# Performance work log

Hardware: AMD Instinct MI355X
Metric: run time of the kernel (lower is better)

The kernel has to match this reference:

```python
import jax, jax.numpy as jnp
import numpy as np

D = 256        # embedding dim (params[0])
V = 50000      # candidate vocab (params[1])
VW = 200000    # word vocab
B = 1024       # number of entities (batched ragged loop)
C = 64         # candidates per side (padded fixed length)
TOP_K = 10     # params[2]


def setup_inputs() -> dict:
    key = jax.random.key(0)
    ks = jax.random.split(key, 10)
    return {
        "word_l_ids": jax.random.randint(ks[0], (B,), 0, VW),
        "word_r_ids": jax.random.randint(ks[1], (B,), 0, VW),
        "cand_l_ids": jax.random.randint(ks[2], (B, C), 0, V),
        "cand_r_ids": jax.random.randint(ks[3], (B, C), 0, V),
        "word_embeds": jax.random.normal(ks[4], (VW, D), dtype=jnp.float32) * 0.1,
        "candidate_embeds": jax.random.normal(ks[5], (V, D), dtype=jnp.float32) * 0.1,
        # truncated_normal(stddev=0.5) for W_a, stddev=1.0 for W_c
        "W_a": jax.random.truncated_normal(ks[6], -2.0, 2.0, (D, D), dtype=jnp.float32) * 0.5,
        "b_a": jnp.zeros((1, D), dtype=jnp.float32),
        "W_c": jax.random.truncated_normal(ks[7], -2.0, 2.0, (2 * D, D), dtype=jnp.float32),
        "b_c": jnp.zeros((1, D), dtype=jnp.float32),
    }


def reference(word_l_ids, word_r_ids, cand_l_ids, cand_r_ids,
              word_embeds, candidate_embeds, W_a, b_a, W_c, b_c):
    # per-entity embedding lookups
    wl = word_embeds[word_l_ids]            # [B, D]
    wr = word_embeds[word_r_ids]            # [B, D]
    cl = candidate_embeds[cand_l_ids]       # [B, C, D]
    cr = candidate_embeds[cand_r_ids]       # [B, C, D]

    def attend(word, cands):
        # embed_word_align = tanh(word @ W_a + b_a)
        align = jnp.tanh(word @ W_a + b_a)                       # [B, D]
        # softmax over candidate axis (axis=0 in original per-entity view)
        scores = jnp.einsum("bcd,bd->bc", cands, align)          # [B, C]
        att = jax.nn.softmax(scores, axis=-1)                    # [B, C]
        # weighted sum of candidate embeddings
        return jnp.einsum("bc,bcd->bd", att, cands)              # [B, D]

    # note: left aggregation attends over RIGHT candidates and vice versa
    aggre_l = attend(wl, cr)
    aggre_r = attend(wr, cl)

    words_whole = wl + wr
    cands_whole = aggre_r + aggre_l
    phrase = jnp.tanh(jnp.concatenate([words_whole, cands_whole], axis=-1) @ W_c + b_c)  # [B, D]

    logits = phrase @ candidate_embeds.T    # [B, V]
    y_pred = jax.nn.softmax(logits, axis=-1)
    _, top_candidates = jax.lax.top_k(y_pred, TOP_K)             # [B, TOP_K]
    return y_pred, top_candidates
```

## Files before the change

kernel.cpp:

```cpp
#include <hip/hip_runtime.h>
#include <math.h>

#define DD 256
#define BB 1024
#define CC 64
#define VV 50000
#define TOPK 10
#define BM 128
#define BN 128
#define BK 64
#define LDK 72
#define NCHUNK 391
#define NMBLK 8
#define NWG (NCHUNK * NMBLK)
#define MAXCAND 60

typedef __attribute__((ext_vector_type(8))) short bf16x8;
typedef __attribute__((ext_vector_type(4))) float f32x4;

__device__ inline unsigned short f2bf(float x) {
    unsigned u = __float_as_uint(x);
    unsigned r = (u + 0x7FFFu + ((u >> 16) & 1u)) >> 16;
    return (unsigned short)r;
}

__global__ __launch_bounds__(256) void k_prep(
    const float* __restrict__ CE, unsigned short* __restrict__ CEb)
{
    const int i = blockIdx.x * 256 + threadIdx.x;
    const size_t base = (size_t)i * 8;
    if (base >= (size_t)VV * DD) return;
    const float4 a = *(const float4*)(CE + base);
    const float4 b = *(const float4*)(CE + base + 4);
    uint4 o;
    o.x = (unsigned)f2bf(a.x) | ((unsigned)f2bf(a.y) << 16);
    o.y = (unsigned)f2bf(a.z) | ((unsigned)f2bf(a.w) << 16);
    o.z = (unsigned)f2bf(b.x) | ((unsigned)f2bf(b.y) << 16);
    o.w = (unsigned)f2bf(b.z) | ((unsigned)f2bf(b.w) << 16);
    *(uint4*)(CEb + base) = o;
}

__global__ __launch_bounds__(256) void k_phrase(
    const int* __restrict__ wl_ids, const int* __restrict__ wr_ids,
    const int* __restrict__ cl_ids, const int* __restrict__ cr_ids,
    const float* __restrict__ WE, const float* __restrict__ CE,
    const float* __restrict__ W_a, const float* __restrict__ b_a,
    const float* __restrict__ W_c, const float* __restrict__ b_c,
    float* __restrict__ phrase, unsigned short* __restrict__ phraseb)
{
    const int b = blockIdx.x;
    const int t = threadIdx.x;
    __shared__ float s_wl[DD], s_wr[DD], s_align[DD], s_agg0[DD], s_agg1[DD];
    __shared__ float s_part[256];
    __shared__ float s_att[CC];
    __shared__ int s_rid[CC];

    s_wl[t] = WE[(size_t)wl_ids[b] * DD + t];
    s_wr[t] = WE[(size_t)wr_ids[b] * DD + t];
    __syncthreads();

    for (int side = 0; side < 2; ++side) {
        const float* w    = (side == 0) ? s_wl : s_wr;
        const int*   cids = (side == 0) ? (cr_ids + b * CC) : (cl_ids + b * CC);

        float acc = b_a[t];
        #pragma unroll 4
        for (int k = 0; k < DD; ++k) acc = fmaf(w[k], W_a[k * DD + t], acc);
        s_align[t] = tanhf(acc);
        if (t < CC) s_rid[t] = cids[t];
        __syncthreads();

        {
            const int c = t & 63, p = t >> 6;
            const float* crow = CE + (size_t)s_rid[c] * DD + p * 64;
            const float* al = s_align + p * 64;
            float sc = 0.f;
            #pragma unroll 4
            for (int j = 0; j < 64; ++j) sc = fmaf(crow[j], al[j], sc);
            s_part[t] = sc;
        }
        __syncthreads();
        if (t < CC) {
            float s = s_part[t] + s_part[64 + t] + s_part[128 + t] + s_part[192 + t];
            float m = s;
            for (int off = 32; off; off >>= 1) m = fmaxf(m, __shfl_xor(m, off, 64));
            float e = expf(s - m);
            float sum = e;
            for (int off = 32; off; off >>= 1) sum += __shfl_xor(sum, off, 64);
            s_att[t] = e / sum;
        }
        __syncthreads();
        {
            float ag = 0.f;
            #pragma unroll 4
            for (int c = 0; c < CC; ++c)
                ag = fmaf(s_att[c], CE[(size_t)s_rid[c] * DD + t], ag);
            if (side == 0) s_agg0[t] = ag; else s_agg1[t] = ag;
        }
        __syncthreads();
    }

    s_wl[t]  += s_wr[t];
    s_agg0[t] += s_agg1[t];
    __syncthreads();

    float acc = b_c[t];
    #pragma unroll 4
    for (int k = 0; k < DD; ++k) acc = fmaf(s_wl[k],  W_c[k * DD + t], acc);
    #pragma unroll 4
    for (int k = 0; k < DD; ++k) acc = fmaf(s_agg0[k], W_c[(DD + k) * DD + t], acc);
    const float ph = tanhf(acc);
    phrase[b * DD + t] = ph;
    phraseb[b * DD + t] = f2bf(ph);
}

__global__ __launch_bounds__(256) void k_align(
    const int* __restrict__ wl_ids, const int* __restrict__ wr_ids,
    const float* __restrict__ WE,
    const float* __restrict__ W_a, const float* __restrict__ b_a,
    float* __restrict__ alignbuf, float* __restrict__ wordsum)
{
    __shared__ float sA[32][260];
    __shared__ int s_id[32];

    const int t  = threadIdx.x;
    const int rt = blockIdx.x >> 2;
    const int cg = blockIdx.x & 3;
    const int b0 = rt * 16;
    const int s0 = rt * 32;

    if (t < 32) {
        const int e = b0 + (t >> 1);
        s_id[t] = (t & 1) ? wr_ids[e] : wl_ids[e];
    }
    __syncthreads();

    #pragma unroll 8
    for (int r = 0; r < 32; ++r)
        sA[r][t] = WE[(size_t)s_id[r] * DD + t];
    __syncthreads();

    if (cg == 0) {
        #pragma unroll
        for (int i = 0; i < 16; ++i)
            wordsum[(size_t)(b0 + i) * DD + t] = sA[2 * i][t] + sA[2 * i + 1][t];
    }

    const int c = t & 63, mg = t >> 6;
    const int col = cg * 64 + c;
    const float ba = b_a[col];
    float acc[8];
    #pragma unroll
    for (int j = 0; j < 8; ++j) acc[j] = ba;

    for (int k4 = 0; k4 < 64; ++k4) {
        const int kb = k4 * 4;
        const float w0 = W_a[(size_t)(kb + 0) * DD + col];
        const float w1 = W_a[(size_t)(kb + 1) * DD + col];
        const float w2 = W_a[(size_t)(kb + 2) * DD + col];
        const float w3 = W_a[(size_t)(kb + 3) * DD + col];
        #pragma unroll
        for (int j = 0; j < 8; ++j) {
            const float4 a = *(const float4*)&sA[mg * 8 + j][kb];
            acc[j] = fmaf(a.x, w0, acc[j]);
            acc[j] = fmaf(a.y, w1, acc[j]);
            acc[j] = fmaf(a.z, w2, acc[j]);
            acc[j] = fmaf(a.w, w3, acc[j]);
        }
    }
    #pragma unroll
    for (int j = 0; j < 8; ++j)
        alignbuf[(size_t)(s0 + mg * 8 + j) * DD + col] = tanhf(acc[j]);
}

__global__ __launch_bounds__(256) void k_attn(
    const int* __restrict__ cl_ids, const int* __restrict__ cr_ids,
    const float* __restrict__ CE, const float* __restrict__ alignbuf,
    float* __restrict__ aggsum)
{
    __shared__ float sC[CC][260];
    __shared__ float sAl[DD];
    __shared__ float s_part[256];
    __shared__ float s_att[CC];
    __shared__ int s_rid[CC];

    const int b = blockIdx.x;
    const int t = threadIdx.x;
    float agg_acc = 0.f;

    for (int side = 0; side < 2; ++side) {
        const int* cids = (side == 0) ? (cr_ids + b * CC) : (cl_ids + b * CC);
        if (t < CC) s_rid[t] = cids[t];
        sAl[t] = alignbuf[(size_t)(2 * b + side) * DD + t];
        __syncthreads();

        #pragma unroll 8
        for (int r = 0; r < CC; ++r)
            sC[r][t] = CE[(size_t)s_rid[r] * DD + t];
        __syncthreads();

        {
            const int c = t & 63, p = t >> 6;
            float sc = 0.f;
            #pragma unroll
            for (int jj = 0; jj < 16; ++jj) {
                const float4 v  = *(const float4*)&sC[c][p * 64 + 4 * jj];
                const float4 al = *(const float4*)&sAl[p * 64 + 4 * jj];
                sc = fmaf(v.x, al.x, sc);
                sc = fmaf(v.y, al.y, sc);
                sc = fmaf(v.z, al.z, sc);
                sc = fmaf(v.w, al.w, sc);
            }
            s_part[t] = sc;
        }
        __syncthreads();
        if (t < CC) {
            float s = s_part[t] + s_part[64 + t] + s_part[128 + t] + s_part[192 + t];
            float m = s;
            for (int off = 32; off; off >>= 1) m = fmaxf(m, __shfl_xor(m, off, 64));
            float e = expf(s - m);
            float sum = e;
            for (int off = 32; off; off >>= 1) sum += __shfl_xor(sum, off, 64);
            s_att[t] = e / sum;
        }
        __syncthreads();
        {
            float ag = 0.f;
            #pragma unroll 8
            for (int c = 0; c < CC; ++c)
                ag = fmaf(s_att[c], sC[c][t], ag);
            agg_acc += ag;
        }
        __syncthreads();
    }
    aggsum[(size_t)b * DD + t] = agg_acc;
}

__global__ __launch_bounds__(256) void k_phrase2(
    const float* __restrict__ wordsum, const float* __restrict__ aggsum,
    const float* __restrict__ W_c, const float* __restrict__ b_c,
    float* __restrict__ phrase, unsigned short* __restrict__ phraseb)
{
    __shared__ float sX[16][516];

    const int t  = threadIdx.x;
    const int rt = blockIdx.x >> 2;
    const int cg = blockIdx.x & 3;
    const int b0 = rt * 16;

    #pragma unroll
    for (int i = 0; i < 16; ++i) {
        sX[i][t]       = wordsum[(size_t)(b0 + i) * DD + t];
        sX[i][DD + t]  = aggsum [(size_t)(b0 + i) * DD + t];
    }
    __syncthreads();

    const int c = t & 63, mg = t >> 6;
    const int col = cg * 64 + c;
    const float bc = b_c[col];
    float acc[4];
    #pragma unroll
    for (int j = 0; j < 4; ++j) acc[j] = bc;

    for (int k4 = 0; k4 < 128; ++k4) {
        const int kb = k4 * 4;
        const float w0 = W_c[(size_t)(kb + 0) * DD + col];
        const float w1 = W_c[(size_t)(kb + 1) * DD + col];
        const float w2 = W_c[(size_t)(kb + 2) * DD + col];
        const float w3 = W_c[(size_t)(kb + 3) * DD + col];
        #pragma unroll
        for (int j = 0; j < 4; ++j) {
            const float4 a = *(const float4*)&sX[mg * 4 + j][kb];
            acc[j] = fmaf(a.x, w0, acc[j]);
            acc[j] = fmaf(a.y, w1, acc[j]);
            acc[j] = fmaf(a.z, w2, acc[j]);
            acc[j] = fmaf(a.w, w3, acc[j]);
        }
    }
    #pragma unroll
    for (int j = 0; j < 4; ++j) {
        const int b = b0 + mg * 4 + j;
        const float ph = tanhf(acc[j]);
        phrase[(size_t)b * DD + col] = ph;
        phraseb[(size_t)b * DD + col] = f2bf(ph);
    }
}

template<bool STATS, bool BF16CE>
__global__ __launch_bounds__(256) void k_gemm(
    const unsigned short* __restrict__ phraseb,
    const float* __restrict__ CE, const unsigned short* __restrict__ CEb,
    float* __restrict__ out,
    float* __restrict__ pmax, float* __restrict__ psum,
    const float* __restrict__ rowM, const float* __restrict__ rowInvS,
    const float* __restrict__ rowTh,
    int* __restrict__ cand_idx, int* __restrict__ cand_cnt)
{
    __shared__ __align__(16) char smem_raw[BM * LDK * 2 * 2];
    unsigned short* sA = (unsigned short*)smem_raw;
    unsigned short* sB = sA + BM * LDK;

    const int t = threadIdx.x;
    const int wave = t >> 6, lane = t & 63;
    const int wm = wave >> 1, wn = wave & 1;
    const int quad = lane >> 4, l15 = lane & 15;

    const int wg = blockIdx.x;
    const int q  = (wg & 7) * NCHUNK + (wg >> 3);
    const int m0 = (q & 7) * BM;
    const int cn = q >> 3;
    const int n0 = cn * BN;

    f32x4 acc[4][4] = {};

    for (int k0 = 0; k0 < DD; k0 += BK) {
        __syncthreads();
        #pragma unroll
        for (int r = 0; r < 4; ++r) {
            const int idx = t + r * 256;
            const int m = idx >> 3, k8 = (idx & 7) * 8;
            const uint4 v = *(const uint4*)(phraseb + (size_t)(m0 + m) * DD + k0 + k8);
            *(uint4*)(sA + m * LDK + k8) = v;
        }
        if constexpr (BF16CE) {
            #pragma unroll
            for (int r = 0; r < 4; ++r) {
                const int idx = t + r * 256;
                const int n = idx >> 3, k8 = (idx & 7) * 8;
                const int gn = n0 + n;
                uint4 v = make_uint4(0u, 0u, 0u, 0u);
                if (gn < VV) v = *(const uint4*)(CEb + (size_t)gn * DD + k0 + k8);
                *(uint4*)(sB + n * LDK + k8) = v;
            }
        } else {
            #pragma unroll
            for (int r = 0; r < 8; ++r) {
                const int idx = t + r * 256;
                const int n = idx >> 4, k4 = (idx & 15) * 4;
                const int gn = n0 + n;
                float4 v = make_float4(0.f, 0.f, 0.f, 0.f);
                if (gn < VV) v = *(const float4*)(CE + (size_t)gn * DD + k0 + k4);
                ushort4 h;
                h.x = f2bf(v.x); h.y = f2bf(v.y); h.z = f2bf(v.z); h.w = f2bf(v.w);
                *(ushort4*)(sB + n * LDK + k4) = h;
            }
        }
        __syncthreads();
        #pragma unroll
        for (int kk = 0; kk < BK; kk += 32) {
            bf16x8 af[4], bfr[4];
            #pragma unroll
            for (int i = 0; i < 4; ++i) {
                af[i]  = *(const bf16x8*)(sA + (wm * 64 + i * 16 + l15) * LDK + kk + quad * 8);
                bfr[i] = *(const bf16x8*)(sB + (wn * 64 + i * 16 + l15) * LDK + kk + quad * 8);
            }
            #pragma unroll
            for (int i = 0; i < 4; ++i)
                #pragma unroll
                for (int j = 0; j < 4; ++j)
                    acc[i][j] = __builtin_amdgcn_mfma_f32_16x16x32_bf16(af[i], bfr[j], acc[i][j], 0, 0, 0);
        }
    }

    bool val[4];
    #pragma unroll
    for (int j = 0; j < 4; ++j) val[j] = (n0 + wn * 64 + j * 16 + l15) < VV;

    if constexpr (STATS) {
        __shared__ float sM[2][BM], sS[2][BM];
        #pragma unroll
        for (int i = 0; i < 4; ++i) {
            #pragma unroll
            for (int r = 0; r < 4; ++r) {
                float m1 = -INFINITY;
                #pragma unroll
                for (int j = 0; j < 4; ++j) if (val[j]) m1 = fmaxf(m1, acc[i][j][r]);
                #pragma unroll
                for (int off = 8; off >= 1; off >>= 1) m1 = fmaxf(m1, __shfl_xor(m1, off, 64));
                float s = 0.f;
                #pragma unroll
                for (int j = 0; j < 4; ++j) if (val[j]) s += __expf(acc[i][j][r] - m1);
                #pragma unroll
                for (int off = 8; off >= 1; off >>= 1) s += __shfl_xor(s, off, 64);
                if (l15 == 0) {
                    const int mloc = wm * 64 + i * 16 + quad * 4 + r;
                    sM[wn][mloc] = m1;
                    sS[wn][mloc] = s;
                }
            }
        }
        __syncthreads();
        if (t < BM) {
            const float Ma = sM[0][t], Mb = sM[1][t];
            const float nM = fmaxf(Ma, Mb);
            const float S  = sS[0][t] * __expf(Ma - nM) + sS[1][t] * __expf(Mb - nM);
            const size_t o = (size_t)(m0 + t) * NCHUNK + cn;
            pmax[o] = nM;
            psum[o] = S;
        }
    } else {
        __shared__ float sMr[BM], sIr[BM], sTr[BM];
        if (t < BM) {
            sMr[t] = rowM[m0 + t];
            sIr[t] = rowInvS[m0 + t];
            sTr[t] = rowTh[m0 + t];
        }
        float* stage = (float*)smem_raw;
        #pragma unroll
        for (int h = 0; h < 4; ++h) {
            __syncthreads();
            if (wm == (h >> 1)) {
                const int ibase = (h & 1) * 2;
                #pragma unroll
                for (int ii = 0; ii < 2; ++ii) {
                    const int i = ibase + ii;
                    #pragma unroll
                    for (int r = 0; r < 4; ++r) {
                        const int ml = wm * 64 + i * 16 + quad * 4 + r;
                        const int rl = ii * 16 + quad * 4 + r;
                        const float M = sMr[ml], inv = sIr[ml], th = sTr[ml];
                        #pragma unroll
                        for (int j = 0; j < 4; ++j) {
                            const float y = __expf(acc[i][j][r] - M) * inv;
                            stage[rl * 132 + wn * 64 + j * 16 + l15] = y;
                            if (val[j] && y >= th) {
                                const int gm = m0 + ml;
                                const int gn = n0 + wn * 64 + j * 16 + l15;
                                const int p = atomicAdd(&cand_cnt[gm], 1);
                                if (p < MAXCAND) cand_idx[gm * MAXCAND + p] = gn;
                            }
                        }
                    }
                }
            }
            __syncthreads();
            #pragma unroll
            for (int k = 0; k < 4; ++k) {
                const int f = t + k * 256;
                const int row = f >> 5, c4 = f & 31;
                const int gcol = n0 + c4 * 4;
                if (gcol + 3 < VV) {
                    const f32x4 v = *(const f32x4*)&stage[row * 132 + c4 * 4];
                    __builtin_nontemporal_store(v,
                        (f32x4*)(out + (size_t)(m0 + h * 32 + row) * VV + gcol));
                }
            }
        }
    }
}

__global__ __launch_bounds__(64) void k_rowstats(
    const float* __restrict__ pmax, const float* __restrict__ psum,
    float* __restrict__ rowM, float* __restrict__ rowInvS, float* __restrict__ rowTh,
    int* __restrict__ cand_cnt)
{
    const int b = blockIdx.x, t = threadIdx.x;
    float M = -INFINITY, S = 0.f;
    float top[TOPK];
    #pragma unroll
    for (int j = 0; j < TOPK; ++j) top[j] = -INFINITY;

    for (int c = t; c < NCHUNK; c += 64) {
        const float m = pmax[(size_t)b * NCHUNK + c];
        const float s = psum[(size_t)b * NCHUNK + c];
        const float nM = fmaxf(M, m);
        S = S * __expf(M - nM) + s * __expf(m - nM);
        M = nM;
        if (m > top[TOPK - 1]) {
            float v = m;
            #pragma unroll
            for (int p = 0; p < TOPK; ++p) {
                const float hi = fmaxf(top[p], v), lo = fminf(top[p], v);
                top[p] = hi; v = lo;
            }
        }
    }
    #pragma unroll
    for (int off = 32; off; off >>= 1) {
        const float m2 = __shfl_xor(M, off, 64);
        const float s2 = __shfl_xor(S, off, 64);
        const float nM = fmaxf(M, m2);
        S = S * __expf(M - nM) + s2 * __expf(m2 - nM);
        M = nM;
    }
    float v10 = -INFINITY;
    for (int k = 0; k < TOPK; ++k) {
        float g = top[0];
        #pragma unroll
        for (int off = 32; off; off >>= 1) g = fmaxf(g, __shfl_xor(g, off, 64));
        v10 = g;
        const unsigned long long mk = __ballot(top[0] == g);
        if (mk && t == __ffsll(mk) - 1) {
            #pragma unroll
            for (int p = 0; p < TOPK - 1; ++p) top[p] = top[p + 1];
            top[TOPK - 1] = -INFINITY;
        }
    }
    if (t == 0) {
        rowM[b] = M;
        const float inv = 1.f / S;
        rowInvS[b] = inv;
        rowTh[b] = 0.90f * __expf(v10 - M) * inv;
        cand_cnt[b] = 0;
    }
}

__global__ __launch_bounds__(64) void k_rescore(
    const float* __restrict__ phrase, const float* __restrict__ CE,
    const int* __restrict__ cand_idx, const int* __restrict__ cand_cnt,
    float* __restrict__ topk_out)
{
    const int b = blockIdx.x, lane = threadIdx.x;
    int cnt = cand_cnt[b];
    if (cnt > MAXCAND) cnt = MAXCAND;
    __shared__ float s_val[MAXCAND];
    __shared__ int   s_idx[MAXCAND];

    if (lane < MAXCAND) { s_val[lane] = -INFINITY; s_idx[lane] = 0x7ffffff0; }
    __syncthreads();

    const float4 ph = *(const float4*)(phrase + (size_t)b * DD + lane * 4);
    for (int c = 0; c < cnt; ++c) {
        const int id = cand_idx[b * MAXCAND + c];
        const float4 ce = *(const float4*)(CE + (size_t)id * DD + lane * 4);
        float d = ph.x * ce.x + ph.y * ce.y + ph.z * ce.z + ph.w * ce.w;
        #pragma unroll
        for (int off = 32; off; off >>= 1) d += __shfl_xor(d, off, 64);
        if (lane == 0) { s_val[c] = d; s_idx[c] = id; }
    }
    __syncthreads();
    if (lane == 0) {
        for (int j = 0; j < TOPK; ++j) {
            int best = j;
            for (int c = j + 1; c < cnt; ++c) {
                if (s_val[c] > s_val[best] ||
                    (s_val[c] == s_val[best] && s_idx[c] < s_idx[best])) best = c;
            }
            const float bv = s_val[best]; const int bi = s_idx[best];
            s_val[best] = s_val[j]; s_idx[best] = s_idx[j];
            s_val[j] = bv; s_idx[j] = bi;
            topk_out[b * TOPK + j] = (float)bi;
        }
    }
}

extern "C" void kernel_launch(void* const* d_in, const int* in_sizes, int n_in,
                              void* d_out, int out_size, void* d_ws, size_t ws_size,
                              hipStream_t stream) {
    const int*   wl_ids = (const int*)d_in[0];
    const int*   wr_ids = (const int*)d_in[1];
    const int*   cl_ids = (const int*)d_in[2];
    const int*   cr_ids = (const int*)d_in[3];
    const float* WE     = (const float*)d_in[4];
    const float* CE     = (const float*)d_in[5];
    const float* W_a    = (const float*)d_in[6];
    const float* b_a    = (const float*)d_in[7];
    const float* W_c    = (const float*)d_in[8];
    const float* b_c    = (const float*)d_in[9];

    float* out = (float*)d_out;
    float* ws  = (float*)d_ws;

    float* phrase  = ws;
    unsigned short* phraseb = (unsigned short*)(ws + 262144);
    float* pmax    = ws + 262144 + 131072;
    float* psum    = pmax + (size_t)BB * NCHUNK;
    float* rowM    = psum + (size_t)BB * NCHUNK;
    float* rowInvS = rowM + BB;
    float* rowTh   = rowInvS + BB;
    int*   cand_idx = (int*)(rowTh + BB);
    int*   cand_cnt = cand_idx + (size_t)BB * MAXCAND;
    float* topk_out = out + (size_t)BB * VV;

    const size_t baseBytes = (size_t)((char*)(cand_cnt + BB) - (char*)ws);

    float* alignbuf = (float*)((char*)ws + baseBytes);
    float* wordsum  = alignbuf + (size_t)2 * BB * DD;
    float* aggsum   = wordsum + (size_t)BB * DD;
    const size_t ext1End = baseBytes + (size_t)4 * BB * DD * 4;
    const bool newphrase = ws_size >= ext1End;

    const size_t ceOff = ((newphrase ? ext1End : baseBytes) + 255) & ~(size_t)255;
    const bool bf16ce = ws_size >= ceOff + (size_t)VV * DD * 2;
    unsigned short* CEb = (unsigned short*)((char*)ws + ceOff);

    if (newphrase) {
        k_align<<<256, 256, 0, stream>>>(wl_ids, wr_ids, WE, W_a, b_a, alignbuf, wordsum);
        k_attn<<<BB, 256, 0, stream>>>(cl_ids, cr_ids, CE, alignbuf, aggsum);
        k_phrase2<<<256, 256, 0, stream>>>(wordsum, aggsum, W_c, b_c, phrase, phraseb);
    } else {
        k_phrase<<<BB, 256, 0, stream>>>(wl_ids, wr_ids, cl_ids, cr_ids,
                                         WE, CE, W_a, b_a, W_c, b_c, phrase, phraseb);
    }
    if (bf16ce) {
        k_prep<<<(VV * DD / 8 + 255) / 256, 256, 0, stream>>>(CE, CEb);
        k_gemm<true, true><<<NWG, 256, 0, stream>>>(phraseb, CE, CEb, out,
            pmax, psum, rowM, rowInvS, rowTh, cand_idx, cand_cnt);
        k_rowstats<<<BB, 64, 0, stream>>>(pmax, psum, rowM, rowInvS, rowTh, cand_cnt);
        k_gemm<false, true><<<NWG, 256, 0, stream>>>(phraseb, CE, CEb, out,
            pmax, psum, rowM, rowInvS, rowTh, cand_idx, cand_cnt);
    } else {
        k_gemm<true, false><<<NWG, 256, 0, stream>>>(phraseb, CE, CEb, out,
            pmax, psum, rowM, rowInvS, rowTh, cand_idx, cand_cnt);
        k_rowstats<<<BB, 64, 0, stream>>>(pmax, psum, rowM, rowInvS, rowTh, cand_cnt);
        k_gemm<false, false><<<NWG, 256, 0, stream>>>(phraseb, CE, CEb, out,
            pmax, psum, rowM, rowInvS, rowTh, cand_idx, cand_cnt);
    }
    k_rescore<<<BB, 64, 0, stream>>>(phrase, CE, cand_idx, cand_cnt, topk_out);
}
```

Before: 642.2 us.

## Replace second GEMM pass with local-max exp write and per-row rescale

The GEMM now runs once. It writes exp(logit - chunk max) to the output along with per-chunk max and sum, and a new k_scale kernel rescales each row in place by exp(chunk max - row max)/S while collecting top-k candidates. This removes the recomputed GEMM but adds a full read and write of the 200MB output. Separately, the attention kernel is split per side, reads candidates straight from global memory instead of staging them in LDS, and stores its result in alignbuf, which removes aggsum.

```diff
diff --git a/kernel.cpp b/kernel.cpp
--- a/kernel.cpp
+++ b/kernel.cpp
@@ -14,6 +14,7 @@
 #define NMBLK 8
 #define NWG (NCHUNK * NMBLK)
 #define MAXCAND 60
+#define QLEN 12500
 
 typedef __attribute__((ext_vector_type(8))) short bf16x8;
 typedef __attribute__((ext_vector_type(4))) float f32x4;
@@ -175,69 +176,59 @@
 
 __global__ __launch_bounds__(256) void k_attn(
     const int* __restrict__ cl_ids, const int* __restrict__ cr_ids,
-    const float* __restrict__ CE, const float* __restrict__ alignbuf,
-    float* __restrict__ aggsum)
-{
-    __shared__ float sC[CC][260];
+    const float* __restrict__ CE, float* __restrict__ alignbuf)
+{
     __shared__ float sAl[DD];
     __shared__ float s_part[256];
     __shared__ float s_att[CC];
     __shared__ int s_rid[CC];
 
-    const int b = blockIdx.x;
+    const int bid = blockIdx.x;
+    const int b = bid >> 1, side = bid & 1;
     const int t = threadIdx.x;
-    float agg_acc = 0.f;
-
-    for (int side = 0; side < 2; ++side) {
-        const int* cids = (side == 0) ? (cr_ids + b * CC) : (cl_ids + b * CC);
-        if (t < CC) s_rid[t] = cids[t];
-        sAl[t] = alignbuf[(size_t)(2 * b + side) * DD + t];
-        __syncthreads();
-
+
+    const int* cids = (side == 0) ? (cr_ids + b * CC) : (cl_ids + b * CC);
+    if (t < CC) s_rid[t] = cids[t];
+    sAl[t] = alignbuf[(size_t)(2 * b + side) * DD + t];
+    __syncthreads();
+
+    {
+        const int c = t & 63, p = t >> 6;
+        const float* crow = CE + (size_t)s_rid[c] * DD + p * 64;
+        float sc = 0.f;
+        #pragma unroll
+        for (int jj = 0; jj < 16; ++jj) {
+            const float4 v  = *(const float4*)(crow + 4 * jj);
+            const float4 al = *(const float4*)&sAl[p * 64 + 4 * jj];
+            sc = fmaf(v.x, al.x, sc);
+            sc = fmaf(v.y, al.y, sc);
+            sc = fmaf(v.z, al.z, sc);
+            sc = fmaf(v.w, al.w, sc);
+        }
+        s_part[t] = sc;
+    }
+    __syncthreads();
+    if (t < CC) {
+        float s = s_part[t] + s_part[64 + t] + s_part[128 + t] + s_part[192 + t];
+        float m = s;
+        for (int off = 32; off; off >>= 1) m = fmaxf(m, __shfl_xor(m, off, 64));
+        float e = expf(s - m);
+        float sum = e;
+        for (int off = 32; off; off >>= 1) sum += __shfl_xor(sum, off, 64);
+        s_att[t] = e / sum;
+    }
+    __syncthreads();
+    {
+        float ag = 0.f;
         #pragma unroll 8
-        for (int r = 0; r < CC; ++r)
-            sC[r][t] = CE[(size_t)s_rid[r] * DD + t];
-        __syncthreads();
-
-        {
-            const int c = t & 63, p = t >> 6;
-            float sc = 0.f;
-            #pragma unroll
-            for (int jj = 0; jj < 16; ++jj) {
-                const float4 v  = *(const float4*)&sC[c][p * 64 + 4 * jj];
-                const float4 al = *(const float4*)&sAl[p * 64 + 4 * jj];
-                sc = fmaf(v.x, al.x, sc);
-                sc = fmaf(v.y, al.y, sc);
-                sc = fmaf(v.z, al.z, sc);
-                sc = fmaf(v.w, al.w, sc);
-            }
-            s_part[t] = sc;
-        }
-        __syncthreads();
-        if (t < CC) {
-            float s = s_part[t] + s_part[64 + t] + s_part[128 + t] + s_part[192 + t];
-            float m = s;
-            for (int off = 32; off; off >>= 1) m = fmaxf(m, __shfl_xor(m, off, 64));
-            float e = expf(s - m);
-            float sum = e;
-            for (int off = 32; off; off >>= 1) sum += __shfl_xor(sum, off, 64);
-            s_att[t] = e / sum;
-        }
-        __syncthreads();
-        {
-            float ag = 0.f;
-            #pragma unroll 8
-            for (int c = 0; c < CC; ++c)
-                ag = fmaf(s_att[c], sC[c][t], ag);
-            agg_acc += ag;
-        }
-        __syncthreads();
-    }
-    aggsum[(size_t)b * DD + t] = agg_acc;
+        for (int c = 0; c < CC; ++c)
+            ag = fmaf(s_att[c], CE[(size_t)s_rid[c] * DD + t], ag);
+        alignbuf[(size_t)(2 * b + side) * DD + t] = ag;
+    }
 }
 
 __global__ __launch_bounds__(256) void k_phrase2(
-    const float* __restrict__ wordsum, const float* __restrict__ aggsum,
+    const float* __restrict__ wordsum, const float* __restrict__ alignbuf,
     const float* __restrict__ W_c, const float* __restrict__ b_c,
     float* __restrict__ phrase, unsigned short* __restrict__ phraseb)
 {
@@ -250,8 +241,9 @@
 
     #pragma unroll
     for (int i = 0; i < 16; ++i) {
-        sX[i][t]       = wordsum[(size_t)(b0 + i) * DD + t];
-        sX[i][DD + t]  = aggsum [(size_t)(b0 + i) * DD + t];
+        sX[i][t]      = wordsum[(size_t)(b0 + i) * DD + t];
+        sX[i][DD + t] = alignbuf[(size_t)(2 * (b0 + i)) * DD + t]
+                      + alignbuf[(size_t)(2 * (b0 + i) + 1) * DD + t];
     }
     __syncthreads();
 
@@ -286,17 +278,15 @@
     }
 }
 
-template<bool STATS, bool BF16CE>
+template<bool BF16CE>
 __global__ __launch_bounds__(256) void k_gemm(
     const unsigned short* __restrict__ phraseb,
     const float* __restrict__ CE, const unsigned short* __restrict__ CEb,
     float* __restrict__ out,
-    float* __restrict__ pmax, float* __restrict__ psum,
-    const float* __restrict__ rowM, const float* __restrict__ rowInvS,
-    const float* __restrict__ rowTh,
-    int* __restrict__ cand_idx, int* __restrict__ cand_cnt)
+    float* __restrict__ pmax, float* __restrict__ psum)
 {
     __shared__ __align__(16) char smem_raw[BM * LDK * 2 * 2];
+    __shared__ float sM[2][BM], sS[2][BM];
     unsigned short* sA = (unsigned short*)smem_raw;
     unsigned short* sB = sA + BM * LDK;
 
@@ -366,84 +356,68 @@
     #pragma unroll
     for (int j = 0; j < 4; ++j) val[j] = (n0 + wn * 64 + j * 16 + l15) < VV;
 
-    if constexpr (STATS) {
-        __shared__ float sM[2][BM], sS[2][BM];
-        #pragma unroll
-        for (int i = 0; i < 4; ++i) {
-            #pragma unroll
-            for (int r = 0; r < 4; ++r) {
-                float m1 = -INFINITY;
+    #pragma unroll
+    for (int i = 0; i < 4; ++i) {
+        #pragma unroll
+        for (int r = 0; r < 4; ++r) {
+            float m1 = -INFINITY;
+            #pragma unroll
+            for (int j = 0; j < 4; ++j) if (val[j]) m1 = fmaxf(m1, acc[i][j][r]);
+            #pragma unroll
+            for (int off = 8; off >= 1; off >>= 1) m1 = fmaxf(m1, __shfl_xor(m1, off, 64));
+            float s = 0.f;
+            #pragma unroll
+            for (int j = 0; j < 4; ++j) if (val[j]) s += __expf(acc[i][j][r] - m1);
+            #pragma unroll
+            for (int off = 8; off >= 1; off >>= 1) s += __shfl_xor(s, off, 64);
+            if (l15 == 0) {
+                const int mloc = wm * 64 + i * 16 + quad * 4 + r;
+                sM[wn][mloc] = m1;
+                sS[wn][mloc] = s;
+            }
+        }
+    }
+    __syncthreads();
+    if (t < BM) {
+        const float Ma = sM[0][t], Mb = sM[1][t];
+        const float nM = fmaxf(Ma, Mb);
+        const float S  = sS[0][t] * __expf(Ma - nM) + sS[1][t] * __expf(Mb - nM);
+        const size_t o = (size_t)(m0 + t) * NCHUNK + cn;
+        pmax[o] = nM;
+        psum[o] = S;
+        sM[0][t] = nM;
+    }
+
+    float* stage = (float*)smem_raw;
+    #pragma unroll
+    for (int h = 0; h < 4; ++h) {
+        __syncthreads();
+        if (wm == (h >> 1)) {
+            const int ibase = (h & 1) * 2;
+            #pragma unroll
+            for (int ii = 0; ii < 2; ++ii) {
+                const int i = ibase + ii;
                 #pragma unroll
-                for (int j = 0; j < 4; ++j) if (val[j]) m1 = fmaxf(m1, acc[i][j][r]);
-                #pragma unroll
-                for (int off = 8; off >= 1; off >>= 1) m1 = fmaxf(m1, __shfl_xor(m1, off, 64));
-                float s = 0.f;
-                #pragma unroll
-                for (int j = 0; j < 4; ++j) if (val[j]) s += __expf(acc[i][j][r] - m1);
-                #pragma unroll
-                for (int off = 8; off >= 1; off >>= 1) s += __shfl_xor(s, off, 64);
-                if (l15 == 0) {
-                    const int mloc = wm * 64 + i * 16 + quad * 4 + r;
-                    sM[wn][mloc] = m1;
-                    sS[wn][mloc] = s;
+                for (int r = 0; r < 4; ++r) {
+                    const int ml = wm * 64 + i * 16 + quad * 4 + r;
+                    const int rl = ii * 16 + quad * 4 + r;
+                    const float mc = sM[0][ml];
+                    #pragma unroll
+                    for (int j = 0; j < 4; ++j)
+                        stage[rl * 132 + wn * 64 + j * 16 + l15] = __expf(acc[i][j][r] - mc);
                 }
             }
         }
         __syncthreads();
-        if (t < BM) {
-            const float Ma = sM[0][t], Mb = sM[1][t];
-            const float nM = fmaxf(Ma, Mb);
-            const float S  = sS[0][t] * __expf(Ma - nM) + sS[1][t] * __expf(Mb - nM);
-            const size_t o = (size_t)(m0 + t) * NCHUNK + cn;
-            pmax[o] = nM;
-            psum[o] = S;
-        }
-    } else {
-        __shared__ float sMr[BM], sIr[BM], sTr[BM];
-        if (t < BM) {
-            sMr[t] = rowM[m0 + t];
-            sIr[t] = rowInvS[m0 + t];
-            sTr[t] = rowTh[m0 + t];
-        }
-        float* stage = (float*)smem_raw;
-        #pragma unroll
-        for (int h = 0; h < 4; ++h) {
-            __syncthreads();
-            if (wm == (h >> 1)) {
-                const int ibase = (h & 1) * 2;
-                #pragma unroll
-                for (int ii = 0; ii < 2; ++ii) {
-                    const int i = ibase + ii;
-                    #pragma unroll
-                    for (int r = 0; r < 4; ++r) {
-                        const int ml = wm * 64 + i * 16 + quad * 4 + r;
-                        const int rl = ii * 16 + quad * 4 + r;
-                        const float M = sMr[ml], inv = sIr[ml], th = sTr[ml];
-                        #pragma unroll
-                        for (int j = 0; j < 4; ++j) {
-                            const float y = __expf(acc[i][j][r] - M) * inv;
-                            stage[rl * 132 + wn * 64 + j * 16 + l15] = y;
-                            if (val[j] && y >= th) {
-                                const int gm = m0 + ml;
-                                const int gn = n0 + wn * 64 + j * 16 + l15;
-                                const int p = atomicAdd(&cand_cnt[gm], 1);
-                                if (p < MAXCAND) cand_idx[gm * MAXCAND + p] = gn;
-                            }
-                        }
-                    }
-                }
-            }
-            __syncthreads();
-            #pragma unroll
-            for (int k = 0; k < 4; ++k) {
-                const int f = t + k * 256;
-                const int row = f >> 5, c4 = f & 31;
-                const int gcol = n0 + c4 * 4;
-                if (gcol + 3 < VV) {
-                    const f32x4 v = *(const f32x4*)&stage[row * 132 + c4 * 4];
-                    __builtin_nontemporal_store(v,
-                        (f32x4*)(out + (size_t)(m0 + h * 32 + row) * VV + gcol));
-                }
+        #pragma unroll
+        for (int k = 0; k < 4; ++k) {
+            const int f = t + k * 256;
+            const int row = f >> 5, c4 = f & 31;
+            const int gcol = n0 + c4 * 4;
+            if (gcol + 3 < VV) {
+                const f32x4 v = *(const f32x4*)&stage[row * 132 + c4 * 4];
+                __builtin_nontemporal_store(v,
+                    (f32x4*)(out + (size_t)(m0 + h * 32 + row) * VV + gcol));
             }
         }
     }
@@ -502,6 +476,38 @@
         rowInvS[b] = inv;
         rowTh[b] = 0.90f * __expf(v10 - M) * inv;
         cand_cnt[b] = 0;
+    }
+}
+
+__global__ __launch_bounds__(256) void k_scale(
+    float* __restrict__ ylog, const float* __restrict__ pmax,
+    const float* __restrict__ rowM, const float* __restrict__ rowInvS,
+    const float* __restrict__ rowTh,
+    int* __restrict__ cand_idx, int* __restrict__ cand_cnt)
+{
+    __shared__ float f[NCHUNK];
+    const int b = blockIdx.x, qq = blockIdx.y, t = threadIdx.x;
+    const float M = rowM[b];
+    const float inv = rowInvS[b];
+    const float th = rowTh[b];
+    for (int c = t; c < NCHUNK; c += 256)
+        f[c] = __expf(pmax[(size_t)b * NCHUNK + c] - M) * inv;
+    __syncthreads();
+
+    float* row = ylog + (size_t)b * VV;
+    const int end = (qq + 1) * QLEN;
+    for (int i = qq * QLEN + t * 4; i < end; i += 1024) {
+        const f32x4 u = *(const f32x4*)(row + i);
+        const float fc = f[i >> 7];
+        const f32x4 y = u * fc;
+        __builtin_nontemporal_store(y, (f32x4*)(row + i));
+        #pragma unroll
+        for (int jj = 0; jj < 4; ++jj) {
+            if (y[jj] >= th) {
+                const int p = atomicAdd(&cand_cnt[b], 1);
+                if (p < MAXCAND) cand_idx[b * MAXCAND + p] = i + jj;
+            }
+        }
     }
 }
 
@@ -576,8 +582,7 @@
 
     float* alignbuf = (float*)((char*)ws + baseBytes);
     float* wordsum  = alignbuf + (size_t)2 * BB * DD;
-    float* aggsum   = wordsum + (size_t)BB * DD;
-    const size_t ext1End = baseBytes + (size_t)4 * BB * DD * 4;
+    const size_t ext1End = baseBytes + (size_t)3 * BB * DD * 4;
     const bool newphrase = ws_size >= ext1End;
 
     const size_t ceOff = ((newphrase ? ext1End : baseBytes) + 255) & ~(size_t)255;
@@ -586,25 +591,20 @@
 
     if (newphrase) {
         k_align<<<256, 256, 0, stream>>>(wl_ids, wr_ids, WE, W_a, b_a, alignbuf, wordsum);
-        k_attn<<<BB, 256, 0, stream>>>(cl_ids, cr_ids, CE, alignbuf, aggsum);
-        k_phrase2<<<256, 256, 0, stream>>>(wordsum, aggsum, W_c, b_c, phrase, phraseb);
+        k_attn<<<2 * BB, 256, 0, stream>>>(cl_ids, cr_ids, CE, alignbuf);
+        k_phrase2<<<256, 256, 0, stream>>>(wordsum, alignbuf, W_c, b_c, phrase, phraseb);
     } else {
         k_phrase<<<BB, 256, 0, stream>>>(wl_ids, wr_ids, cl_ids, cr_ids,
                                          WE, CE, W_a, b_a, W_c, b_c, phrase, phraseb);
     }
     if (bf16ce) {
         k_prep<<<(VV * DD / 8 + 255) / 256, 256, 0, stream>>>(CE, CEb);
-        k_gemm<true, true><<<NWG, 256, 0, stream>>>(phraseb, CE, CEb, out,
-            pmax, psum, rowM, rowInvS, rowTh, cand_idx, cand_cnt);
-        k_rowstats<<<BB, 64, 0, stream>>>(pmax, psum, rowM, rowInvS, rowTh, cand_cnt);
-        k_gemm<false, true><<<NWG, 256, 0, stream>>>(phraseb, CE, CEb, out,
-            pmax, psum, rowM, rowInvS, rowTh, cand_idx, cand_cnt);
+        k_gemm<true><<<NWG, 256, 0, stream>>>(phraseb, CE, CEb, out, pmax, psum);
     } else {
-        k_gemm<true, false><<<NWG, 256, 0, stream>>>(phraseb, CE, CEb, out,
-            pmax, psum, rowM, rowInvS, rowTh, cand_idx, cand_cnt);
-        k_rowstats<<<BB, 64, 0, stream>>>(pmax, psum, rowM, rowInvS, rowTh, cand_cnt);
-        k_gemm<false, false><<<NWG, 256, 0, stream>>>(phraseb, CE, CEb, out,
-            pmax, psum, rowM, rowInvS, rowTh, cand_idx, cand_cnt);
-    }
+        k_gemm<false><<<NWG, 256, 0, stream>>>(phraseb, CE, CEb, out, pmax, psum);
+    }
+    k_rowstats<<<BB, 64, 0, stream>>>(pmax, psum, rowM, rowInvS, rowTh, cand_cnt);
+    k_scale<<<dim3(BB, 4), 256, 0, stream>>>(out, pmax, rowM, rowInvS, rowTh,
+                                             cand_idx, cand_cnt);
     k_rescore<<<BB, 64, 0, stream>>>(phrase, CE, cand_idx, cand_cnt, topk_out);
 }
```

Measured after the change: 689.6 us. 1.07x slower.
